# Optimization experiments

Measured on AMD Instinct MI355X. Metric: run time of the kernel, lower is better.

The kernel has to match this reference:

```python
import jax, jax.numpy as jnp
import numpy as np

N_NODES = 100000
N_EDGES = 3200000
F_IN = 128
CHANNELS = 128


def setup_inputs() -> dict:
    key = jax.random.key(0)
    k1, k2, k3, k4, k5 = jax.random.split(key, 5)
    x = jax.random.normal(k1, (N_NODES, F_IN), dtype=jnp.float32)
    kernel = jax.random.normal(k2, (F_IN, CHANNELS), dtype=jnp.float32) * (1.0 / np.sqrt(F_IN))
    bias = jnp.zeros((CHANNELS,), dtype=jnp.float32)
    edge_row = jnp.sort(jax.random.randint(k3, (N_EDGES,), 0, N_NODES, dtype=jnp.int32))
    edge_col = jax.random.randint(k4, (N_EDGES,), 0, N_NODES, dtype=jnp.int32)
    edge_val = jax.random.uniform(k5, (N_EDGES,), dtype=jnp.float32)
    return {"x": x, "kernel": kernel, "bias": bias, "edge_val": edge_val,
            "edge_row": edge_row, "edge_col": edge_col}


def reference(x, kernel, bias, edge_val, edge_row, edge_col):
    # Z = relu(A_tilde @ (X @ W) + b), A_tilde given in COO form (row, col, val)
    n = x.shape[0]
    xw = x @ kernel                              # [N, C] dense projection
    msgs = xw[edge_col] * edge_val[:, None]      # [E, C] gather + scale
    agg = jax.ops.segment_sum(msgs, edge_row, num_segments=n)  # SpMM scatter
    return jax.nn.relu(agg + bias)
```

## Files before the change

### kernel.cpp

```cpp
#include <hip/hip_runtime.h>

#define F_IN 128
#define CH   128

typedef __attribute__((ext_vector_type(8))) short bf16x8;
typedef __attribute__((ext_vector_type(4))) float f32x4;
typedef __attribute__((ext_vector_type(2))) float f32x2;
typedef __attribute__((ext_vector_type(4))) unsigned u32x4;

static __device__ __forceinline__ ushort f2b(float f) {
  union { float f; unsigned u; } v; v.f = f;
  const unsigned u = v.u;
  return (ushort)((u + 0x7FFFu + ((u >> 16) & 1u)) >> 16);
}

__global__ __launch_bounds__(512) void gemm_rowptr_fused(
    const float* __restrict__ x, const float* __restrict__ w,
    unsigned char* __restrict__ xwq, float* __restrict__ scale,
    const int* __restrict__ edge_row, int* __restrict__ row_ptr,
    int n, int n_edges, int gemm_blocks) {
  __shared__ __align__(16) ushort Wt[F_IN * CH];
  const int t = threadIdx.x;

  if ((int)blockIdx.x >= gemm_blocks) {
    const int r = ((int)blockIdx.x - gemm_blocks) * 512 + t;
    if (r <= n) {
      int lo = 0, hi = n_edges;
      while (lo < hi) {
        const int mid = (lo + hi) >> 1;
        if (edge_row[mid] < r) lo = mid + 1; else hi = mid;
      }
      row_ptr[r] = lo;
    }
    return;
  }

  for (int i = t; i < (F_IN * CH) / 4; i += 512) {
    const int k  = i >> 5;
    const int n4 = (i & 31) << 2;
    const f32x4 wv = *(const f32x4*)&w[k * CH + n4];
#pragma unroll
    for (int q = 0; q < 4; ++q) {
      const int nn = n4 + q;
      const int byte = (nn * 256 + k * 2) ^ ((nn & 7) << 4);
      *(ushort*)((char*)Wt + byte) = f2b(wv[q]);
    }
  }
  __syncthreads();

  const int wave = t >> 6, lane = t & 63;
  const int R0   = blockIdx.x * 128 + wave * 16;
  const int arow = R0 + (lane & 15);
  const int kgrp = (lane >> 4) * 8;

  bf16x8 a[4];
#pragma unroll
  for (int s = 0; s < 4; ++s) {
    if (arow < n) {
      const f32x4 p0 = __builtin_nontemporal_load(
          (const f32x4*)&x[arow * F_IN + s * 32 + kgrp]);
      const f32x4 p1 = __builtin_nontemporal_load(
          (const f32x4*)&x[arow * F_IN + s * 32 + kgrp + 4]);
#pragma unroll
      for (int j = 0; j < 4; ++j) {
        a[s][j]     = (short)f2b(p0[j]);
        a[s][j + 4] = (short)f2b(p1[j]);
      }
    } else {
#pragma unroll
      for (int j = 0; j < 8; ++j) a[s][j] = (short)0;
    }
  }

  f32x4 acc[8];
#pragma unroll
  for (int t8 = 0; t8 < 8; ++t8) acc[t8] = (f32x4){0.f, 0.f, 0.f, 0.f};

#pragma unroll
  for (int t8 = 0; t8 < 8; ++t8) {
    const int col = t8 * 16 + (lane & 15);
#pragma unroll
    for (int s = 0; s < 4; ++s) {
      const int byte = (col * 256 + (s * 32 + kgrp) * 2) ^ ((col & 7) << 4);
      const bf16x8 b = *(const bf16x8*)((const char*)Wt + byte);
      acc[t8] = __builtin_amdgcn_mfma_f32_16x16x32_bf16(a[s], b, acc[t8], 0, 0, 0);
    }
  }

  const int li = lane & 15;
  const int r0 = R0 + (lane >> 4) * 4;
#pragma unroll
  for (int i = 0; i < 4; ++i) {
    const int rr = r0 + i;
    float m = 0.f;
#pragma unroll
    for (int t8 = 0; t8 < 8; ++t8) m = fmaxf(m, fabsf(acc[t8][i]));
    m = fmaxf(m, __shfl_xor(m, 1));
    m = fmaxf(m, __shfl_xor(m, 2));
    m = fmaxf(m, __shfl_xor(m, 4));
    m = fmaxf(m, __shfl_xor(m, 8));
    const float inv = (m > 1e-20f) ? 127.f / m : 0.f;
    if (rr < n) {
      if (li == 0) scale[rr] = m * (1.f / 127.f);
#pragma unroll
      for (int t8 = 0; t8 < 8; ++t8) {
        const float q = rintf(acc[t8][i] * inv) + 128.f;
        xwq[rr * CH + t8 * 16 + li] = (unsigned char)q;
      }
    }
  }
}

#define ACCD(word, j0)                                                  \
  do {                                                                  \
    f32x2 lo, hi;                                                       \
    lo[0] = (float)((word) & 0xFFu);                                    \
    lo[1] = (float)(((word) >> 8) & 0xFFu);                             \
    hi[0] = (float)(((word) >> 16) & 0xFFu);                            \
    hi[1] = (float)((word) >> 24);                                      \
    acc2[(j0)]     = __builtin_elementwise_fma(vv, lo, acc2[(j0)]);     \
    acc2[(j0) + 1] = __builtin_elementwise_fma(vv, hi, acc2[(j0) + 1]); \
  } while (0)

#define ACC16PK(U, V)                                                   \
  do {                                                                  \
    const f32x2 vv = {(V), (V)};                                        \
    ACCD((U)[0], 0);                                                    \
    ACCD((U)[1], 2);                                                    \
    ACCD((U)[2], 4);                                                    \
    ACCD((U)[3], 6);                                                    \
  } while (0)

__global__ __launch_bounds__(256) void spmm_rowwave(
    const unsigned char* __restrict__ xwq, const float* __restrict__ scale,
    const float* __restrict__ edge_val, const int* __restrict__ edge_col,
    const int* __restrict__ row_ptr, const float* __restrict__ bias,
    float* __restrict__ out, int n) {
  const int wid = (int)((blockIdx.x * blockDim.x + threadIdx.x) >> 6);
  if (wid >= n) return;
  const int lane = threadIdx.x & 63;
  const int g8 = lane >> 3;
  const int l8 = lane & 7;
  const int start = row_ptr[wid], end = row_ptr[wid + 1];
  const u32x4* __restrict__ xw4 = (const u32x4*)xwq;

  f32x2 acc2[8];
#pragma unroll
  for (int j = 0; j < 8; ++j) acc2[j] = (f32x2){0.f, 0.f};
  float S = 0.f;

  for (int e0 = start; e0 < end; e0 += 64) {
    const int e = e0 + lane;
    int   c_my = 0;
    float vp_my = 0.f;
    if (e < end) {
      c_my = __builtin_nontemporal_load(edge_col + e);
      const float v = __builtin_nontemporal_load(edge_val + e);
      vp_my = v * scale[c_my];
    }
    S += vp_my;

    u32x4 u[8];
    float vp[8];
#pragma unroll
    for (int it = 0; it < 8; ++it) {
      const int src = it * 8 + g8;
      const int c   = __shfl(c_my, src);
      vp[it] = __shfl(vp_my, src);
      u[it]  = xw4[c * 8 + l8];
    }

#pragma unroll
    for (int it = 0; it < 8; ++it) {
      if (e0 + it * 8 >= end) break;
      ACC16PK(u[it], vp[it]);
    }
  }

  S += __shfl_xor(S, 1);
  S += __shfl_xor(S, 2);
  S += __shfl_xor(S, 4);
  S += __shfl_xor(S, 8);
  S += __shfl_xor(S, 16);
  S += __shfl_xor(S, 32);

  float* acc = (float*)acc2;
#pragma unroll
  for (int j = 0; j < 16; ++j) {
    acc[j] += __shfl_xor(acc[j], 8);
    acc[j] += __shfl_xor(acc[j], 16);
    acc[j] += __shfl_xor(acc[j], 32);
  }

  if (g8 == 0) {
    const int c = l8 * 16;
    const float off = 128.f * S;
#pragma unroll
    for (int q = 0; q < 4; ++q) {
      const f32x4 bv = *(const f32x4*)&bias[c + q * 4];
      f32x4 o;
      o[0] = fmaxf(acc[q * 4 + 0] - off + bv[0], 0.f);
      o[1] = fmaxf(acc[q * 4 + 1] - off + bv[1], 0.f);
      o[2] = fmaxf(acc[q * 4 + 2] - off + bv[2], 0.f);
      o[3] = fmaxf(acc[q * 4 + 3] - off + bv[3], 0.f);
      __builtin_nontemporal_store(o, (f32x4*)&out[(size_t)wid * CH + c + q * 4]);
    }
  }
}

extern "C" void kernel_launch(void* const* d_in, const int* in_sizes, int n_in,
                              void* d_out, int out_size, void* d_ws, size_t ws_size,
                              hipStream_t stream) {
  const float* x        = (const float*)d_in[0];
  const float* kernel   = (const float*)d_in[1];
  const float* bias     = (const float*)d_in[2];
  const float* edge_val = (const float*)d_in[3];
  const int*   edge_row = (const int*)d_in[4];
  const int*   edge_col = (const int*)d_in[5];
  float* out = (float*)d_out;

  const int n       = in_sizes[0] / F_IN;
  const int n_edges = in_sizes[3];

  unsigned char* xwq = (unsigned char*)d_ws;
  float* scale = (float*)((char*)d_ws + (size_t)n * CH);
  int* rowptr  = (int*)((char*)d_ws + (size_t)n * CH + (size_t)n * sizeof(float));

  const int GB = (n + 127) / 128;
  const int RB = (n + 1 + 511) / 512;
  gemm_rowptr_fused<<<GB + RB, 512, 0, stream>>>(x, kernel, xwq, scale,
                                                 edge_row, rowptr,
                                                 n, n_edges, GB);

  spmm_rowwave<<<(n + 3) / 4, 256, 0, stream>>>(xwq, scale, edge_val, edge_col,
                                                rowptr, bias, out, n);
}
```

Baseline: 127.3 us.

## Process two rows per wavefront in SpMM with fast path for short rows

Each wavefront now handles a pair of adjacent rows. When both rows have at most 64 edges, it issues all gathers for both rows before accumulating, so more loads are in flight per wave and half as many waves are launched. Rows with more edges fall back to the old per-row loop. The cost is higher register pressure from holding 16 gathered vectors, which may reduce occupancy, plus an extra branch.

```diff
diff --git a/kernel.cpp b/kernel.cpp
--- a/kernel.cpp
+++ b/kernel.cpp
@@ -111,39 +111,63 @@
   }
 }
 
-#define ACCD(word, j0)                                                  \
-  do {                                                                  \
-    f32x2 lo, hi;                                                       \
-    lo[0] = (float)((word) & 0xFFu);                                    \
-    lo[1] = (float)(((word) >> 8) & 0xFFu);                             \
-    hi[0] = (float)(((word) >> 16) & 0xFFu);                            \
-    hi[1] = (float)((word) >> 24);                                      \
-    acc2[(j0)]     = __builtin_elementwise_fma(vv, lo, acc2[(j0)]);     \
-    acc2[(j0) + 1] = __builtin_elementwise_fma(vv, hi, acc2[(j0) + 1]); \
+#define ACCD(A2, word, j0, vv)                                            \
+  do {                                                                    \
+    f32x2 lo_, hi_;                                                       \
+    lo_[0] = (float)((word) & 0xFFu);                                     \
+    lo_[1] = (float)(((word) >> 8) & 0xFFu);                              \
+    hi_[0] = (float)(((word) >> 16) & 0xFFu);                             \
+    hi_[1] = (float)((word) >> 24);                                       \
+    (A2)[(j0)]     = __builtin_elementwise_fma(vv, lo_, (A2)[(j0)]);      \
+    (A2)[(j0) + 1] = __builtin_elementwise_fma(vv, hi_, (A2)[(j0) + 1]);  \
   } while (0)
 
-#define ACC16PK(U, V)                                                   \
-  do {                                                                  \
-    const f32x2 vv = {(V), (V)};                                        \
-    ACCD((U)[0], 0);                                                    \
-    ACCD((U)[1], 2);                                                    \
-    ACCD((U)[2], 4);                                                    \
-    ACCD((U)[3], 6);                                                    \
+#define ACC16PK(A2, U, V)                                                 \
+  do {                                                                    \
+    const f32x2 vv_ = {(V), (V)};                                         \
+    ACCD(A2, (U)[0], 0, vv_);                                             \
+    ACCD(A2, (U)[1], 2, vv_);                                             \
+    ACCD(A2, (U)[2], 4, vv_);                                             \
+    ACCD(A2, (U)[3], 6, vv_);                                             \
   } while (0)
 
-__global__ __launch_bounds__(256) void spmm_rowwave(
-    const unsigned char* __restrict__ xwq, const float* __restrict__ scale,
+static __device__ __forceinline__ void reduce_store(
+    f32x2* acc2, float S, const float* __restrict__ bias,
+    float* __restrict__ out, int row, int g8, int l8) {
+  S += __shfl_xor(S, 1);
+  S += __shfl_xor(S, 2);
+  S += __shfl_xor(S, 4);
+  S += __shfl_xor(S, 8);
+  S += __shfl_xor(S, 16);
+  S += __shfl_xor(S, 32);
+  float* acc = (float*)acc2;
+#pragma unroll
+  for (int j = 0; j < 16; ++j) {
+    acc[j] += __shfl_xor(acc[j], 8);
+    acc[j] += __shfl_xor(acc[j], 16);
+    acc[j] += __shfl_xor(acc[j], 32);
+  }
+  if (g8 == 0) {
+    const int c = l8 * 16;
+    const float off = 128.f * S;
+#pragma unroll
+    for (int q = 0; q < 4; ++q) {
+      const f32x4 bv = *(const f32x4*)&bias[c + q * 4];
+      f32x4 o;
+      o[0] = fmaxf(acc[q * 4 + 0] - off + bv[0], 0.f);
+      o[1] = fmaxf(acc[q * 4 + 1] - off + bv[1], 0.f);
+      o[2] = fmaxf(acc[q * 4 + 2] - off + bv[2], 0.f);
+      o[3] = fmaxf(acc[q * 4 + 3] - off + bv[3], 0.f);
+      __builtin_nontemporal_store(o, (f32x4*)&out[(size_t)row * CH + c + q * 4]);
+    }
+  }
+}
+
+static __device__ __forceinline__ void spmm_row_slow(
+    const u32x4* __restrict__ xw4, const float* __restrict__ scale,
     const float* __restrict__ edge_val, const int* __restrict__ edge_col,
-    const int* __restrict__ row_ptr, const float* __restrict__ bias,
-    float* __restrict__ out, int n) {
-  const int wid = (int)((blockIdx.x * blockDim.x + threadIdx.x) >> 6);
-  if (wid >= n) return;
-  const int lane = threadIdx.x & 63;
-  const int g8 = lane >> 3;
-  const int l8 = lane & 7;
-  const int start = row_ptr[wid], end = row_ptr[wid + 1];
-  const u32x4* __restrict__ xw4 = (const u32x4*)xwq;
-
+    const float* __restrict__ bias, float* __restrict__ out,
+    int row, int start, int end, int lane, int g8, int l8) {
   f32x2 acc2[8];
 #pragma unroll
   for (int j = 0; j < 8; ++j) acc2[j] = (f32x2){0.f, 0.f};
@@ -161,50 +185,94 @@
     S += vp_my;
 
     u32x4 u[8];
-    float vp[8];
-#pragma unroll
-    for (int it = 0; it < 8; ++it) {
-      const int src = it * 8 + g8;
-      const int c   = __shfl(c_my, src);
-      vp[it] = __shfl(vp_my, src);
-      u[it]  = xw4[c * 8 + l8];
-    }
-
+#pragma unroll
+    for (int it = 0; it < 8; ++it) {
+      const int c = __shfl(c_my, it * 8 + g8);
+      u[it] = xw4[c * 8 + l8];
+    }
 #pragma unroll
     for (int it = 0; it < 8; ++it) {
       if (e0 + it * 8 >= end) break;
-      ACC16PK(u[it], vp[it]);
-    }
-  }
-
-  S += __shfl_xor(S, 1);
-  S += __shfl_xor(S, 2);
-  S += __shfl_xor(S, 4);
-  S += __shfl_xor(S, 8);
-  S += __shfl_xor(S, 16);
-  S += __shfl_xor(S, 32);
-
-  float* acc = (float*)acc2;
-#pragma unroll
-  for (int j = 0; j < 16; ++j) {
-    acc[j] += __shfl_xor(acc[j], 8);
-    acc[j] += __shfl_xor(acc[j], 16);
-    acc[j] += __shfl_xor(acc[j], 32);
-  }
-
-  if (g8 == 0) {
-    const int c = l8 * 16;
-    const float off = 128.f * S;
-#pragma unroll
-    for (int q = 0; q < 4; ++q) {
-      const f32x4 bv = *(const f32x4*)&bias[c + q * 4];
-      f32x4 o;
-      o[0] = fmaxf(acc[q * 4 + 0] - off + bv[0], 0.f);
-      o[1] = fmaxf(acc[q * 4 + 1] - off + bv[1], 0.f);
-      o[2] = fmaxf(acc[q * 4 + 2] - off + bv[2], 0.f);
-      o[3] = fmaxf(acc[q * 4 + 3] - off + bv[3], 0.f);
-      __builtin_nontemporal_store(o, (f32x4*)&out[(size_t)wid * CH + c + q * 4]);
-    }
+      const float vp = __shfl(vp_my, it * 8 + g8);
+      ACC16PK(acc2, u[it], vp);
+    }
+  }
+  reduce_store(acc2, S, bias, out, row, g8, l8);
+}
+
+__global__ __launch_bounds__(256) void spmm_rowwave2(
+    const unsigned char* __restrict__ xwq, const float* __restrict__ scale,
+    const float* __restrict__ edge_val, const int* __restrict__ edge_col,
+    const int* __restrict__ row_ptr, const float* __restrict__ bias,
+    float* __restrict__ out, int n) {
+  const int pair = (int)((blockIdx.x * blockDim.x + threadIdx.x) >> 6);
+  const int rA = pair * 2;
+  if (rA >= n) return;
+  const int rB = rA + 1;
+  const bool okB = (rB < n);
+  const int lane = threadIdx.x & 63;
+  const int g8 = lane >> 3;
+  const int l8 = lane & 7;
+  const u32x4* __restrict__ xw4 = (const u32x4*)xwq;
+
+  const int sA = row_ptr[rA], eA = row_ptr[rA + 1];
+  const int sB = okB ? row_ptr[rB] : 0;
+  const int eB = okB ? row_ptr[rB + 1] : 0;
+  const int dA = eA - sA, dB = eB - sB;
+
+  if (dA <= 64 && dB <= 64) {
+    int cA = 0; float vpA = 0.f;
+    if (lane < dA) {
+      const int e = sA + lane;
+      cA = __builtin_nontemporal_load(edge_col + e);
+      vpA = __builtin_nontemporal_load(edge_val + e) * scale[cA];
+    }
+    int cB = 0; float vpB = 0.f;
+    if (lane < dB) {
+      const int e = sB + lane;
+      cB = __builtin_nontemporal_load(edge_col + e);
+      vpB = __builtin_nontemporal_load(edge_val + e) * scale[cB];
+    }
+
+    u32x4 uA[8], uB[8];
+#pragma unroll
+    for (int it = 0; it < 8; ++it) {
+      const int c = __shfl(cA, it * 8 + g8);
+      uA[it] = xw4[c * 8 + l8];
+    }
+#pragma unroll
+    for (int it = 0; it < 8; ++it) {
+      const int c = __shfl(cB, it * 8 + g8);
+      uB[it] = xw4[c * 8 + l8];
+    }
+
+    f32x2 accA[8];
+#pragma unroll
+    for (int j = 0; j < 8; ++j) accA[j] = (f32x2){0.f, 0.f};
+#pragma unroll
+    for (int it = 0; it < 8; ++it) {
+      if (it * 8 >= dA) break;
+      const float vp = __shfl(vpA, it * 8 + g8);
+      ACC16PK(accA, uA[it], vp);
+    }
+    reduce_store(accA, vpA, bias, out, rA, g8, l8);
+
+    f32x2 accB[8];
+#pragma unroll
+    for (int j = 0; j < 8; ++j) accB[j] = (f32x2){0.f, 0.f};
+#pragma unroll
+    for (int it = 0; it < 8; ++it) {
+      if (it * 8 >= dB) break;
+      const float vp = __shfl(vpB, it * 8 + g8);
+      ACC16PK(accB, uB[it], vp);
+    }
+    if (okB) reduce_store(accB, vpB, bias, out, rB, g8, l8);
+  } else {
+    spmm_row_slow(xw4, scale, edge_val, edge_col, bias, out, rA, sA, eA,
+                  lane, g8, l8);
+    if (okB)
+      spmm_row_slow(xw4, scale, edge_val, edge_col, bias, out, rB, sB, eB,
+                    lane, g8, l8);
   }
 }
 
@@ -232,6 +300,8 @@
                                                  edge_row, rowptr,
                                                  n, n_edges, GB);
 
-  spmm_rowwave<<<(n + 3) / 4, 256, 0, stream>>>(xwq, scale, edge_val, edge_col,
-                                                rowptr, bias, out, n);
-}
+  const int pairs  = (n + 1) / 2;
+  const int blocks = (pairs + 3) / 4;
+  spmm_rowwave2<<<blocks, 256, 0, stream>>>(xwq, scale, edge_val, edge_col,
+                                            rowptr, bias, out, n);
+}
```

Result: slower. 142.0 us (+11.5%).
